# Performance work log

Hardware: AMD Instinct MI355X
Metric: run time of the kernel (lower is better)

## Reference

```python
import jax, jax.numpy as jnp
import numpy as np

# Mamba2 hyperparams derived from init_kwargs
D_MODEL = 512
FF = 2048
D_STATE = 128
D_CONV = 4
EXPAND = 2
D_INNER = EXPAND * D_MODEL          # 1024
HEADDIM = 64                        # mamba_ssm Mamba2 default
NHEADS = D_INNER // HEADDIM         # 16
NGROUPS = 1                         # default
CONV_DIM = D_INNER + 2 * NGROUPS * D_STATE      # 1280
D_IN_PROJ = 2 * D_INNER + 2 * NGROUPS * D_STATE + NHEADS  # 2320
B_SZ = 2
SEQ = 2048


def setup_inputs() -> dict:
    key = jax.random.key(0)
    ks = jax.random.split(key, 10)
    s = 0.02
    return dict(
        tgt=jax.random.normal(ks[0], (B_SZ, SEQ, D_MODEL), jnp.float32),
        W_in=jax.random.normal(ks[1], (D_MODEL, D_IN_PROJ), jnp.float32) * s,
        conv_w=jax.random.normal(ks[2], (CONV_DIM, D_CONV), jnp.float32) * s,
        conv_b=jnp.zeros((CONV_DIM,), jnp.float32),
        dt_bias=jax.random.uniform(ks[3], (NHEADS,), jnp.float32, -4.0, -1.0),
        A_log=jnp.log(jax.random.uniform(ks[4], (NHEADS,), jnp.float32, 1.0, 16.0)),
        D_skip=jnp.ones((NHEADS,), jnp.float32),
        gnorm_w=jnp.ones((D_INNER,), jnp.float32),
        W_out=jax.random.normal(ks[5], (D_INNER, D_MODEL), jnp.float32) * s,
        n1_g=jnp.ones((D_MODEL,), jnp.float32), n1_b=jnp.zeros((D_MODEL,), jnp.float32),
        ffn_w1=jax.random.normal(ks[6], (D_MODEL, FF), jnp.float32) * s,
        ffn_b1=jnp.zeros((FF,), jnp.float32),
        ffn_w2=jax.random.normal(ks[7], (FF, D_MODEL), jnp.float32) * s,
        ffn_b2=jnp.zeros((D_MODEL,), jnp.float32),
        n3_g=jnp.ones((D_MODEL,), jnp.float32), n3_b=jnp.zeros((D_MODEL,), jnp.float32),
    )


def _layernorm(x, g, b, eps=1e-5):
    m = jnp.mean(x, -1, keepdims=True)
    v = jnp.var(x, -1, keepdims=True)
    return (x - m) * jax.lax.rsqrt(v + eps) * g + b


def _mamba2(x, W_in, conv_w, conv_b, dt_bias, A_log, D_skip, gnorm_w, W_out):
    Bb, S, _ = x.shape
    zxbcdt = x @ W_in                               # (B,S,2320)
    z = zxbcdt[..., :D_INNER]                       # gate (B,S,1024)
    xBC = zxbcdt[..., D_INNER:D_INNER + CONV_DIM]   # (B,S,1280)
    dt = zxbcdt[..., D_INNER + CONV_DIM:]           # (B,S,H)
    # causal depthwise conv1d (kernel D_CONV) + SiLU
    xc = jnp.moveaxis(xBC, 1, 2)                    # (B,C,S)
    xp = jnp.pad(xc, ((0, 0), (0, 0), (D_CONV - 1, 0)))
    yc = sum(conv_w[None, :, k:k + 1] * xp[:, :, k:k + S] for k in range(D_CONV))
    xBC = jax.nn.silu(jnp.moveaxis(yc, 1, 2) + conv_b)
    xs = xBC[..., :D_INNER].reshape(Bb, S, NHEADS, HEADDIM)   # (B,S,H,P)
    Bc = xBC[..., D_INNER:D_INNER + D_STATE]                  # (B,S,N)
    Cc = xBC[..., D_INNER + D_STATE:]                         # (B,S,N)
    dt = jax.nn.softplus(dt + dt_bias)                        # (B,S,H)
    A = -jnp.exp(A_log)                                       # (H,)
    dA = jnp.exp(dt * A)                                      # (B,S,H)
    tm = lambda a: jnp.moveaxis(a, 1, 0)                      # time-major

    def step(h, inp):
        # h: (B,H,P,N) selective state
        dA_t, dt_t, B_t, C_t, x_t = inp
        h = h * dA_t[:, :, None, None] \
            + (dt_t[:, :, None] * x_t)[..., None] * B_t[:, None, None, :]
        y_t = jnp.einsum('bhpn,bn->bhp', h, C_t)
        return h, y_t

    h0 = jnp.zeros((Bb, NHEADS, HEADDIM, D_STATE), x.dtype)
    _, ys = jax.lax.scan(step, h0, (tm(dA), tm(dt), tm(Bc), tm(Cc), tm(xs)))
    y = jnp.moveaxis(ys, 0, 1) + D_skip[None, None, :, None] * xs
    y = y.reshape(Bb, S, D_INNER)
    # gated RMSNorm (norm_before_gate=False): norm(y * silu(z)) * w
    y = y * jax.nn.silu(z)
    y = y * jax.lax.rsqrt(jnp.mean(y * y, -1, keepdims=True) + 1e-5) * gnorm_w
    return y @ W_out


def reference(tgt, W_in, conv_w, conv_b, dt_bias, A_log, D_skip, gnorm_w, W_out,
              n1_g, n1_b, ffn_w1, ffn_b1, ffn_w2, ffn_b2, n3_g, n3_b):
    t = tgt + _mamba2(tgt, W_in, conv_w, conv_b, dt_bias, A_log, D_skip, gnorm_w, W_out)
    t = _layernorm(t, n1_g, n1_b)
    h = jax.nn.gelu(t @ ffn_w1 + ffn_b1, approximate=False) @ ffn_w2 + ffn_b2
    return _layernorm(t + h, n3_g, n3_b)
```

## Files before the change

### kernel.cpp

```cpp
#include <hip/hip_runtime.h>
#include <hip/hip_bf16.h>
#include <cstddef>
#include <cstdint>

#define D_MODEL   512
#define FF        2048
#define D_STATE   128
#define D_INNER   1024
#define HEADDIM   64
#define NHEADS    16
#define CONV_DIM  1280
#define D_IN_PROJ 2320
#define NPJ_PAD   2432
#define B_SZ      2
#define SEQ       2048
#define NTOK      (B_SZ*SEQ)
#define LCH       32
#define NCHUNK    (SEQ/LCH)
#define NCID      (B_SZ*NHEADS*NCHUNK)
#define LN_SLICE  ((size_t)NTOK*D_MODEL)

typedef __attribute__((ext_vector_type(8))) short short8;
typedef __attribute__((ext_vector_type(4))) float f32x4;

__device__ __forceinline__ float sigmoid_f(float x){ return 1.0f/(1.0f+expf(-x)); }
__device__ __forceinline__ float gelu_f(float x){ return 0.5f*x*(1.0f+erff(x*0.70710678118654752f)); }

__device__ __forceinline__ unsigned short bf16bits(float f){
  __hip_bfloat16 h = __float2bfloat16(f);
  return *reinterpret_cast<unsigned short*>(&h);
}
__device__ __forceinline__ float bf2f(unsigned short u){ return __uint_as_float(((unsigned)u)<<16); }
__device__ __forceinline__ float blo(unsigned u){ return __uint_as_float(u<<16); }
__device__ __forceinline__ float bhi(unsigned u){ return __uint_as_float(u & 0xffff0000u); }
__device__ __forceinline__ unsigned bfpack2(float a, float b){
  return (unsigned)bf16bits(a) | ((unsigned)bf16bits(b)<<16);
}

__device__ __forceinline__ void gload16(const void* g, void* l){
  __builtin_amdgcn_global_load_lds((const __attribute__((address_space(1))) void*)g,
                                   (__attribute__((address_space(3))) void*)l, 16, 0, 0);
}

union U4S8 { uint4 v; unsigned short s[8]; };

template<int EPI, typename OT>
__global__ __launch_bounds__(256)
void gemm128(const __hip_bfloat16* __restrict__ A, const __hip_bfloat16* __restrict__ Bt,
             const float* __restrict__ bias, OT* __restrict__ C,
             int N, int K, int ldc)
{
  __shared__ char AsRaw[128*128];
  __shared__ char BsRaw[128*128];

  const int t    = threadIdx.x;
  const int bm   = blockIdx.y * 128;
  const int bn   = blockIdx.x * 128;
  const int lane = t & 63;
  const int wid  = t >> 6;
  const int wr   = wid >> 1;
  const int wc   = wid & 1;
  const int lrow = lane & 15;
  const int lkb  = (lane >> 4) * 16;
  const int sw   = (lrow & 7) << 4;

  const int rA  = t >> 3;
  const int cbA = (t & 7) * 16;
  const int scb = cbA ^ ((rA & 7) << 4);
  const size_t strideA = (size_t)K * 2;
  const char* aSrc = (const char*)A  + (size_t)(bm + rA) * strideA + scb;
  const char* bSrc = (const char*)Bt + (size_t)(bn + rA) * strideA + scb;
  char* aDst = AsRaw + wid * 1024;
  char* bDst = BsRaw + wid * 1024;

  f32x4 acc[4][4];
  #pragma unroll
  for (int m=0;m<4;m++)
    #pragma unroll
    for (int n=0;n<4;n++) acc[m][n] = (f32x4){0.f,0.f,0.f,0.f};

  const char* ArP = AsRaw + (wr*64 + lrow) * 128;
  const char* BrP = BsRaw + (wc*64 + lrow) * 128;

  for (int k0 = 0; k0 < K; k0 += 64) {
    const size_t ko = (size_t)k0 * 2;
    gload16(aSrc + ko,               aDst);
    gload16(aSrc + ko + 32*strideA,  aDst + 4096);
    gload16(aSrc + ko + 64*strideA,  aDst + 8192);
    gload16(aSrc + ko + 96*strideA,  aDst + 12288);
    gload16(bSrc + ko,               bDst);
    gload16(bSrc + ko + 32*strideA,  bDst + 4096);
    gload16(bSrc + ko + 64*strideA,  bDst + 8192);
    gload16(bSrc + ko + 96*strideA,  bDst + 12288);
    __syncthreads();
    #pragma unroll
    for (int kk = 0; kk < 2; ++kk) {
      const int kb = (kk*64 + lkb) ^ sw;
      short8 a0 = *(const short8*)(ArP + 0*2048 + kb);
      short8 a1 = *(const short8*)(ArP + 1*2048 + kb);
      short8 a2 = *(const short8*)(ArP + 2*2048 + kb);
      short8 a3 = *(const short8*)(ArP + 3*2048 + kb);
      short8 b0 = *(const short8*)(BrP + 0*2048 + kb);
      short8 b1 = *(const short8*)(BrP + 1*2048 + kb);
      short8 b2 = *(const short8*)(BrP + 2*2048 + kb);
      short8 b3 = *(const short8*)(BrP + 3*2048 + kb);
      #pragma unroll
      for (int m=0;m<4;m++){
        short8 am = (m==0)?a0:(m==1)?a1:(m==2)?a2:a3;
        acc[m][0] = __builtin_amdgcn_mfma_f32_16x16x32_bf16(am, b0, acc[m][0], 0,0,0);
        acc[m][1] = __builtin_amdgcn_mfma_f32_16x16x32_bf16(am, b1, acc[m][1], 0,0,0);
        acc[m][2] = __builtin_amdgcn_mfma_f32_16x16x32_bf16(am, b2, acc[m][2], 0,0,0);
        acc[m][3] = __builtin_amdgcn_mfma_f32_16x16x32_bf16(am, b3, acc[m][3], 0,0,0);
      }
    }
    __syncthreads();
  }

  const int orow0 = bm + wr*64 + (lane >> 4) * 4;
  const int ocol0 = bn + wc*64 + lrow;
  #pragma unroll
  for (int n=0;n<4;n++) {
    const int col = ocol0 + n*16;
    if (col >= N) continue;
    const float bv = (EPI>=1) ? bias[col] : 0.f;
    #pragma unroll
    for (int m=0;m<4;m++) {
      #pragma unroll
      for (int j=0;j<4;j++) {
        float v = acc[m][n][j] + bv;
        if (EPI==2) v = gelu_f(v);
        OT* cp = C + (size_t)(orow0 + m*16 + j)*ldc + col;
        if constexpr (sizeof(OT)==2) *cp = __float2bfloat16(v); else *cp = v;
      }
    }
  }
}

template<int EPI, typename OT>
__global__ __launch_bounds__(256)
void gemm_bf16(const __hip_bfloat16* __restrict__ A, const __hip_bfloat16* __restrict__ Bt,
               const float* __restrict__ bias, OT* __restrict__ C,
               int N, int K, int ldc, int M, int nsplit)
{
  __shared__ char AsRaw[128*128];
  __shared__ char BsRaw[64*128];

  const int t    = threadIdx.x;
  const int bm   = blockIdx.y * 128;
  const int bn   = blockIdx.x * 64;
  const int z    = blockIdx.z;
  const int Kloop= K / nsplit;
  A += (size_t)z * Kloop;
  Bt += (size_t)z * Kloop;
  C += (size_t)z * M * ldc;

  const int lane = t & 63;
  const int wid  = t >> 6;
  const int wr   = wid >> 1;
  const int wc   = wid & 1;
  const int lrow = lane & 15;
  const int lkb  = (lane >> 4) * 16;
  const int sw   = (lrow & 7) << 4;

  const int rA  = t >> 3;
  const int cbA = (t & 7) * 16;
  const int scb = cbA ^ ((rA & 7) << 4);
  const size_t strideA = (size_t)K * 2;
  const char* aSrc = (const char*)A  + (size_t)(bm + rA) * strideA + scb;
  const char* bSrc = (const char*)Bt + (size_t)(bn + rA) * strideA + scb;
  char* aDst = AsRaw + wid * 1024;
  char* bDst = BsRaw + wid * 1024;

  f32x4 acc[4][2];
  #pragma unroll
  for (int m=0;m<4;m++)
    #pragma unroll
    for (int n=0;n<2;n++) acc[m][n] = (f32x4){0.f,0.f,0.f,0.f};

  const char* ArP = AsRaw + (wr*64 + lrow) * 128;
  const char* BrP = BsRaw + (wc*32 + lrow) * 128;

  for (int k0 = 0; k0 < Kloop; k0 += 64) {
    const size_t ko = (size_t)k0 * 2;
    gload16(aSrc + ko,               aDst);
    gload16(aSrc + ko + 32*strideA,  aDst + 4096);
    gload16(aSrc + ko + 64*strideA,  aDst + 8192);
    gload16(aSrc + ko + 96*strideA,  aDst + 12288);
    gload16(bSrc + ko,               bDst);
    gload16(bSrc + ko + 32*strideA,  bDst + 4096);
    __syncthreads();
    #pragma unroll
    for (int kk = 0; kk < 2; ++kk) {
      const int kb = (kk*64 + lkb) ^ sw;
      short8 a0 = *(const short8*)(ArP + 0*2048 + kb);
      short8 a1 = *(const short8*)(ArP + 1*2048 + kb);
      short8 a2 = *(const short8*)(ArP + 2*2048 + kb);
      short8 a3 = *(const short8*)(ArP + 3*2048 + kb);
      short8 b0 = *(const short8*)(BrP + 0*2048 + kb);
      short8 b1 = *(const short8*)(BrP + 1*2048 + kb);
      acc[0][0] = __builtin_amdgcn_mfma_f32_16x16x32_bf16(a0, b0, acc[0][0], 0,0,0);
      acc[1][0] = __builtin_amdgcn_mfma_f32_16x16x32_bf16(a1, b0, acc[1][0], 0,0,0);
      acc[2][0] = __builtin_amdgcn_mfma_f32_16x16x32_bf16(a2, b0, acc[2][0], 0,0,0);
      acc[3][0] = __builtin_amdgcn_mfma_f32_16x16x32_bf16(a3, b0, acc[3][0], 0,0,0);
      acc[0][1] = __builtin_amdgcn_mfma_f32_16x16x32_bf16(a0, b1, acc[0][1], 0,0,0);
      acc[1][1] = __builtin_amdgcn_mfma_f32_16x16x32_bf16(a1, b1, acc[1][1], 0,0,0);
      acc[2][1] = __builtin_amdgcn_mfma_f32_16x16x32_bf16(a2, b1, acc[2][1], 0,0,0);
      acc[3][1] = __builtin_amdgcn_mfma_f32_16x16x32_bf16(a3, b1, acc[3][1], 0,0,0);
    }
    __syncthreads();
  }

  const int orow0 = bm + wr*64 + (lane >> 4) * 4;
  const int ocol0 = bn + wc*32 + lrow;
  #pragma unroll
  for (int n=0;n<2;n++) {
    const int col = ocol0 + n*16;
    if (col >= N) continue;
    const float bv = (EPI>=1 && z==0) ? bias[col] : 0.f;
    #pragma unroll
    for (int m=0;m<4;m++) {
      #pragma unroll
      for (int j=0;j<4;j++) {
        float v = acc[m][n][j] + bv;
        if (EPI==2) v = gelu_f(v);
        OT* cp = C + (size_t)(orow0 + m*16 + j)*ldc + col;
        if constexpr (sizeof(OT)==2) *cp = __float2bfloat16(v); else *cp = v;
      }
    }
  }
}

__device__ __forceinline__ void tr_tile(const float* __restrict__ in,
                                        __hip_bfloat16* __restrict__ out,
                                        int K, int N, int Npad, int bx, int by)
{
  __shared__ float tbuf[32][33];
  const int tx = threadIdx.x & 31, ty = threadIdx.x >> 5;
  #pragma unroll
  for (int u=0;u<4;u++){
    int k = by*32 + ty + u*8;
    int n = bx*32 + tx;
    tbuf[ty+u*8][tx] = (n < N) ? in[(size_t)k*N + n] : 0.f;
  }
  __syncthreads();
  #pragma unroll
  for (int u=0;u<4;u++){
    int n = bx*32 + ty + u*8;
    int k = by*32 + tx;
    if (n < Npad) out[(size_t)n*K + k] = __float2bfloat16(tbuf[tx][ty+u*8]);
  }
}

__global__ __launch_bounds__(256)
void prep_all(const float* __restrict__ tgt, __hip_bfloat16* __restrict__ tgt_bf,
              const float* __restrict__ W_in,  __hip_bfloat16* __restrict__ Wint,
              const float* __restrict__ W_out, __hip_bfloat16* __restrict__ Woutt,
              const float* __restrict__ W1,    __hip_bfloat16* __restrict__ W1t,
              const float* __restrict__ W2,    __hip_bfloat16* __restrict__ W2t)
{
  int bid = blockIdx.x;
  if (bid < 2048) {
    int i = bid*1024 + threadIdx.x*4;
    float4 v = *(const float4*)(tgt + i);
    *(uint2*)(tgt_bf + i) = (uint2){bfpack2(v.x,v.y), bfpack2(v.z,v.w)};
    return;
  }
  bid -= 2048;
  if (bid < 76*16) { tr_tile(W_in, Wint, D_MODEL, D_IN_PROJ, NPJ_PAD, bid%76, bid/76); return; }
  bid -= 76*16;
  if (bid < 16*32) { tr_tile(W_out, Woutt, D_INNER, D_MODEL, D_MODEL, bid%16, bid/16); return; }
  bid -= 16*32;
  if (bid < 64*16) { tr_tile(W1, W1t, D_MODEL, FF, FF, bid%64, bid/64); return; }
  bid -= 64*16;
  tr_tile(W2, W2t, FF, D_MODEL, D_MODEL, bid%16, bid/16);
}

__global__ __launch_bounds__(256)
void conv_silu(const __hip_bfloat16* __restrict__ zx, const float* __restrict__ cw,
               const float* __restrict__ cb, __hip_bfloat16* __restrict__ xbc)
{
  const int c  = blockIdx.x*256 + threadIdx.x;
  const int t0 = blockIdx.y*64;
  const int b  = blockIdx.z;
  const float w0=cw[c*4+0], w1=cw[c*4+1], w2=cw[c*4+2], w3=cw[c*4+3];
  const float cbv = cb[c];
  const __hip_bfloat16* base = zx + ((size_t)(b*SEQ + t0))*D_IN_PROJ + D_INNER + c;
  __hip_bfloat16* obase = xbc + ((size_t)(b*SEQ + t0))*CONV_DIM + c;
  float xm3, xm2, xm1;
  if (t0 == 0) { xm3 = 0.f; xm2 = 0.f; xm1 = 0.f; }
  else {
    xm3 = __bfloat162float(base[-3*(ptrdiff_t)D_IN_PROJ]);
    xm2 = __bfloat162float(base[-2*(ptrdiff_t)D_IN_PROJ]);
    xm1 = __bfloat162float(base[-1*(ptrdiff_t)D_IN_PROJ]);
  }
  #pragma unroll 4
  for (int t=0; t<64; ++t) {
    float xc = __bfloat162float(base[(size_t)t*D_IN_PROJ]);
    float acc = cbv + w0*xm3 + w1*xm2 + w2*xm1 + w3*xc;
    obase[(size_t)t*CONV_DIM] = __float2bfloat16(acc * sigmoid_f(acc));
    xm3 = xm2; xm2 = xm1; xm1 = xc;
  }
}

__global__ __launch_bounds__(256)
void chunk_intra(const __hip_bfloat16* __restrict__ xbc, const __hip_bfloat16* __restrict__ zx,
                 const float* __restrict__ dt_bias,
                 const float* __restrict__ A_log, const float* __restrict__ D_skip,
                 __hip_bfloat16* __restrict__ y, __hip_bfloat16* __restrict__ Sbuf,
                 float* __restrict__ lcend, float* __restrict__ scl)
{
  __shared__ char sm[38912];
  __shared__ float s_dt[LCH], s_lc[LCH], s_wend[LCH];
  char* Cb  = sm;
  char* Bb  = sm + 8704;
  char* Btb = sm + 17408;
  char* Xtb = sm + 29696;
  char* Mb  = sm + 35840;

  const int cid = blockIdx.x;
  const int c  = cid & (NCHUNK-1);
  const int bh = cid >> 6;
  const int h  = bh & 15;
  const int b  = bh >> 4;
  const int tid = threadIdx.x;
  const int t0 = c*LCH;
  const __hip_bfloat16* rowbase = xbc + ((size_t)(b*SEQ + t0))*CONV_DIM;

  if (tid < 32) {
    float A_h = -expf(A_log[h]);
    float x = __bfloat162float(zx[(size_t)(b*SEQ + t0 + tid)*D_IN_PROJ + (D_INNER + CONV_DIM) + h])
              + dt_bias[h];
    float dtv = (x > 20.f) ? x : log1pf(expf(x));
    float lc = dtv * A_h;
    #pragma unroll
    for (int d=1; d<32; d<<=1) {
      float o = __shfl_up(lc, d, 32);
      if (tid >= d) lc += o;
    }
    float lc31 = __shfl(lc, 31, 32);
    s_dt[tid] = dtv;
    s_lc[tid] = lc;
    s_wend[tid] = expf(lc31 - lc) * dtv;
    scl[cid*LCH + tid] = expf(lc);
    if (tid == 31) lcend[cid] = lc;
  }

  #pragma unroll
  for (int u=0; u<2; ++u) {
    int q = tid + 256*u;
    int r = q >> 4, c8 = (q & 15)*8;
    const __hip_bfloat16* rp = rowbase + (size_t)r*CONV_DIM + D_INNER;
    *(uint4*)(Bb + r*272 + c8*2) = *(const uint4*)(rp + c8);
    *(uint4*)(Cb + r*272 + c8*2) = *(const uint4*)(rp + D_STATE + c8);
  }
  {
    int j = tid >> 3, p0 = (tid & 7)*8;
    U4S8 xv; xv.v = *(const uint4*)(rowbase + (size_t)j*CONV_DIM + h*HEADDIM + p0);
    #pragma unroll
    for (int k=0;k<8;k++)
      *(unsigned short*)(Xtb + ((p0+k)*48 + j)*2) = xv.s[k];
  }
  __syncthreads();

  #pragma unroll
  for (int u=0; u<2; ++u) {
    int q = tid + 256*u;
    int j = q >> 4, n8 = (q & 15)*8;
    const float w = s_wend[j];
    U4S8 bv; bv.v = *(const uint4*)(Bb + j*272 + n8*2);
    #pragma unroll
    for (int k=0;k<8;k++)
      *(unsigned short*)(Btb + ((n8+k)*48 + j)*2) = bf16bits(bf2f(bv.s[k]) * w);
  }

  const int lane = tid & 63;
  const int w    = tid >> 6;
  const int lrow = lane & 15;
  const int lkb  = (lane >> 4) * 16;
  {
    const int wi = w >> 1, wj = w & 1;
    f32x4 g = (f32x4){0.f,0.f,0.f,0.f};
    const char* Ar = Cb + (wi*16 + lrow)*272 + lkb;
    const char* Br = Bb + (wj*16 + lrow)*272 + lkb;
    #pragma unroll
    for (int ks=0; ks<4; ks++){
      short8 a  = *(const short8*)(Ar + ks*64);
      short8 bb = *(const short8*)(Br + ks*64);
      g = __builtin_amdgcn_mfma_f32_16x16x32_bf16(a, bb, g, 0,0,0);
    }
    const int j = wj*16 + lrow;
    const float lcj = s_lc[j], dtj = s_dt[j];
    const float dsk = D_skip[h];
    const int i0 = wi*16 + (lane>>4)*4;
    #pragma unroll
    for (int r=0;r<4;r++){
      int i = i0 + r;
      float m = 0.f;
      if (j <= i) { m = g[r]*expf(s_lc[i]-lcj)*dtj; if (j==i) m += dsk; }
      *(unsigned short*)(Mb + (i*48 + j)*2) = bf16bits(m);
    }
  }
  __syncthreads();

  {
    const int it = w >> 1;
    const int pb = (w & 1)*2;
    short8 am = *(const short8*)(Mb + (it*16+lrow)*96 + lkb);
    __hip_bfloat16* ybase = y + ((size_t)(b*SEQ+t0))*D_INNER + h*HEADDIM;
    #pragma unroll
    for (int pi=0; pi<2; pi++){
      short8 xv = *(const short8*)(Xtb + ((pb+pi)*16+lrow)*96 + lkb);
      f32x4 ya = __builtin_amdgcn_mfma_f32_16x16x32_bf16(am, xv, (f32x4){0.f,0.f,0.f,0.f}, 0,0,0);
      #pragma unroll
      for (int r=0;r<4;r++){
        int i = it*16 + (lane>>4)*4 + r;
        ybase[(size_t)i*D_INNER + (pb+pi)*16 + lrow] = __float2bfloat16(ya[r]);
      }
    }
  }

  f32x4 sacc[8];
  {
    short8 ax = *(const short8*)(Xtb + (w*16+lrow)*96 + lkb);
    #pragma unroll
    for (int nt=0;nt<8;nt++){
      short8 bv = *(const short8*)(Btb + (nt*16+lrow)*96 + lkb);
      sacc[nt] = __builtin_amdgcn_mfma_f32_16x16x32_bf16(ax, bv, (f32x4){0.f,0.f,0.f,0.f}, 0,0,0);
    }
  }
  __syncthreads();
  {
    const int p0b = w*16 + (lane>>4)*4;
    #pragma unroll
    for (int nt=0;nt<8;nt++){
      int n = nt*16 + lrow;
      #pragma unroll
      for (int r=0;r<4;r++)
        *(unsigned short*)(sm + (p0b+r)*272 + n*2) = bf16bits(sacc[nt][r]);
    }
  }
  __syncthreads();
  __hip_bfloat16* Sout = Sbuf + (size_t)cid*(D_STATE*HEADDIM);
  #pragma unroll
  for (int u=0;u<4;u++){
    int q = tid*4+u, row = q>>4, c8 = (q&15)*8;
    *(uint4*)(Sout + row*128 + c8) = *(const uint4*)(sm + row*272 + c8*2);
  }
}

__global__ __launch_bounds__(256)
void state_scan(__hip_bfloat16* __restrict__ Sbuf, const float* __restrict__ lcend)
{
  const int bh = blockIdx.x >> 2;
  const int sl = blockIdx.x & 3;
  const int tid = threadIdx.x;
  uint4* Sb4 = (uint4*)Sbuf;
  const int idx0 = bh*NCHUNK*1024 + sl*256 + tid;

  float H[8];
  #pragma unroll
  for (int r=0;r<8;r++) H[r]=0.f;
  uint4 cur = Sb4[idx0];
  uint4 nx1 = Sb4[idx0 + 1024];
  float lc0 = lcend[bh*NCHUNK];
  float lc1 = lcend[bh*NCHUNK + 1];
  for (int c=0;c<NCHUNK;c++){
    uint4 nx2; float lc2;
    if (c + 2 < NCHUNK) { nx2 = Sb4[idx0 + (c+2)*1024]; lc2 = lcend[bh*NCHUNK + c + 2]; }
    else                { nx2 = make_uint4(0,0,0,0);    lc2 = 0.f; }
    float e = expf(lc0);
    uint4 o;
    o.x = bfpack2(H[0],H[1]); o.y = bfpack2(H[2],H[3]);
    o.z = bfpack2(H[4],H[5]); o.w = bfpack2(H[6],H[7]);
    Sb4[idx0 + c*1024] = o;
    H[0]=e*H[0]+blo(cur.x); H[1]=e*H[1]+bhi(cur.x);
    H[2]=e*H[2]+blo(cur.y); H[3]=e*H[3]+bhi(cur.y);
    H[4]=e*H[4]+blo(cur.z); H[5]=e*H[5]+bhi(cur.z);
    H[6]=e*H[6]+blo(cur.w); H[7]=e*H[7]+bhi(cur.w);
    cur = nx1; nx1 = nx2; lc0 = lc1; lc1 = lc2;
  }
}

__global__ __launch_bounds__(256)
void chunk_inter(const __hip_bfloat16* __restrict__ xbc, const __hip_bfloat16* __restrict__ Sbuf,
                 const float* __restrict__ scl, __hip_bfloat16* __restrict__ y)
{
  __shared__ char sm2[8704 + 17408];
  __shared__ float s_scl[LCH];
  char* Cb = sm2;
  char* Ht = sm2 + 8704;
  const int cid = blockIdx.x;
  const int c  = cid & (NCHUNK-1);
  const int bh = cid >> 6;
  const int h  = bh & 15;
  const int b  = bh >> 4;
  const int tid = threadIdx.x;
  const int t0 = c*LCH;
  const __hip_bfloat16* rowbase = xbc + ((size_t)(b*SEQ + t0))*CONV_DIM;

  #pragma unroll
  for (int u=0;u<2;u++){
    int q = tid + 256*u;
    int r = q >> 4, c8 = (q & 15)*8;
    *(uint4*)(Cb + r*272 + c8*2) = *(const uint4*)(rowbase + (size_t)r*CONV_DIM + D_INNER + D_STATE + c8);
  }
  const uint4* Hin = (const uint4*)(Sbuf + (size_t)cid*(D_STATE*HEADDIM));
  #pragma unroll
  for (int u=0;u<4;u++){
    int q = tid*4+u, row = q>>4, c8 = (q&15)*8;
    *(uint4*)(Ht + row*272 + c8*2) = Hin[q];
  }
  if (tid < 32) s_scl[tid] = scl[cid*LCH + tid];
  __syncthreads();

  const int lane = tid & 63;
  const int w    = tid >> 6;
  const int lrow = lane & 15;
  const int lkb  = (lane >> 4) * 16;
  const int it   = w >> 1;
  const int pb   = (w & 1)*2;
  f32x4 acc[2];
  acc[0] = (f32x4){0.f,0.f,0.f,0.f};
  acc[1] = (f32x4){0.f,0.f,0.f,0.f};
  const char* Ar = Cb + (it*16+lrow)*272 + lkb;
  const char* H0 = Ht + ((pb+0)*16+lrow)*272 + lkb;
  const char* H1 = Ht + ((pb+1)*16+lrow)*272 + lkb;
  #pragma unroll
  for (int ks=0; ks<4; ks++){
    short8 a  = *(const short8*)(Ar + ks*64);
    short8 h0 = *(const short8*)(H0 + ks*64);
    short8 h1 = *(const short8*)(H1 + ks*64);
    acc[0] = __builtin_amdgcn_mfma_f32_16x16x32_bf16(a, h0, acc[0], 0,0,0);
    acc[1] = __builtin_amdgcn_mfma_f32_16x16x32_bf16(a, h1, acc[1], 0,0,0);
  }
  __hip_bfloat16* ybase = y + ((size_t)(b*SEQ+t0))*D_INNER + h*HEADDIM;
  #pragma unroll
  for (int pi=0; pi<2; pi++){
    #pragma unroll
    for (int r=0;r<4;r++){
      int i = it*16 + (lane>>4)*4 + r;
      __hip_bfloat16* yp = ybase + (size_t)i*D_INNER + (pb+pi)*16 + lrow;
      float v = __bfloat162float(*yp) + s_scl[i]*acc[pi][r];
      *yp = __float2bfloat16(v);
    }
  }
}

__global__ __launch_bounds__(256)
void gate_rms(const __hip_bfloat16* __restrict__ zx, const float* __restrict__ gw,
              const __hip_bfloat16* __restrict__ yin, __hip_bfloat16* __restrict__ ybf)
{
  int tok = blockIdx.x;
  int c = threadIdx.x*4;
  uint2 zv2 = *(const uint2*)(zx + (size_t)tok*D_IN_PROJ + c);
  uint2 yv2 = *(const uint2*)(yin + (size_t)tok*D_INNER + c);
  float z0 = blo(zv2.x), z1 = bhi(zv2.x), z2 = blo(zv2.y), z3 = bhi(zv2.y);
  float y0 = blo(yv2.x), y1 = bhi(yv2.x), y2 = blo(yv2.y), y3 = bhi(yv2.y);
  float g0 = y0 * (z0 * sigmoid_f(z0));
  float g1 = y1 * (z1 * sigmoid_f(z1));
  float g2 = y2 * (z2 * sigmoid_f(z2));
  float g3 = y3 * (z3 * sigmoid_f(z3));
  float ss = g0*g0 + g1*g1 + g2*g2 + g3*g3;
  #pragma unroll
  for (int m=32;m>=1;m>>=1) ss += __shfl_xor(ss, m, 64);
  __shared__ float red[4];
  int wv = threadIdx.x >> 6;
  if ((threadIdx.x & 63)==0) red[wv]=ss;
  __syncthreads();
  float tot = red[0]+red[1]+red[2]+red[3];
  float sc = rsqrtf(tot*(1.f/1024.f) + 1e-5f);
  float4 gwv = *(const float4*)(gw + c);
  *(uint2*)(ybf + (size_t)tok*D_INNER + c) =
      (uint2){bfpack2(g0*sc*gwv.x, g1*sc*gwv.y), bfpack2(g2*sc*gwv.z, g3*sc*gwv.w)};
}

template<int WBF, int NS>
__global__ __launch_bounds__(256)
void add_ln(const float* __restrict__ a, const float* __restrict__ bres,
            const float* __restrict__ gg, const float* __restrict__ bb,
            float* __restrict__ out, __hip_bfloat16* __restrict__ outbf)
{
  int tok = blockIdx.x;
  size_t o = (size_t)tok*D_MODEL;
  int c0 = threadIdx.x, c1 = threadIdx.x + 256;
  float v0 = bres[o+c0];
  float v1 = bres[o+c1];
  #pragma unroll
  for (int z=0; z<NS; ++z) {
    v0 += a[o + z*LN_SLICE + c0];
    v1 += a[o + z*LN_SLICE + c1];
  }
  float s = v0+v1, sq = v0*v0+v1*v1;
  #pragma unroll
  for (int m=32;m>=1;m>>=1){ s += __shfl_xor(s,m,64); sq += __shfl_xor(sq,m,64); }
  __shared__ float rs[4], rq[4];
  int wv = threadIdx.x>>6;
  if ((threadIdx.x&63)==0){ rs[wv]=s; rq[wv]=sq; }
  __syncthreads();
  float S = rs[0]+rs[1]+rs[2]+rs[3];
  float Q = rq[0]+rq[1]+rq[2]+rq[3];
  float mean = S*(1.f/512.f);
  float var  = Q*(1.f/512.f) - mean*mean;
  float inv  = rsqrtf(var + 1e-5f);
  float o0 = (v0-mean)*inv*gg[c0] + bb[c0];
  float o1 = (v1-mean)*inv*gg[c1] + bb[c1];
  out[o+c0] = o0;
  out[o+c1] = o1;
  if (WBF) { outbf[o+c0] = __float2bfloat16(o0); outbf[o+c1] = __float2bfloat16(o1); }
}

extern "C" void kernel_launch(void* const* d_in, const int* in_sizes, int n_in,
                              void* d_out, int out_size, void* d_ws, size_t ws_size,
                              hipStream_t stream)
{
  const float* tgt    = (const float*)d_in[0];
  const float* W_in   = (const float*)d_in[1];
  const float* conv_w = (const float*)d_in[2];
  const float* conv_b = (const float*)d_in[3];
  const float* dt_bias= (const float*)d_in[4];
  const float* A_log  = (const float*)d_in[5];
  const float* D_skip = (const float*)d_in[6];
  const float* gnorm_w= (const float*)d_in[7];
  const float* W_out  = (const float*)d_in[8];
  const float* n1_g   = (const float*)d_in[9];
  const float* n1_b   = (const float*)d_in[10];
  const float* ffn_w1 = (const float*)d_in[11];
  const float* ffn_b1 = (const float*)d_in[12];
  const float* ffn_w2 = (const float*)d_in[13];
  const float* ffn_b2 = (const float*)d_in[14];
  const float* n3_g   = (const float*)d_in[15];
  const float* n3_b   = (const float*)d_in[16];
  float* out = (float*)d_out;
  float* ws  = (float*)d_ws;

  float* zxF  = ws;
  __hip_bfloat16* zx = (__hip_bfloat16*)zxF;
  float* xbcF = zxF + (size_t)NTOK*D_IN_PROJ;
  __hip_bfloat16* xbc = (__hip_bfloat16*)xbcF;
  float* ybF  = xbcF + 2621440 + 65536;
  __hip_bfloat16* yb = (__hip_bfloat16*)ybF;
  float* Sreg = ybF + 4194304;
  __hip_bfloat16* Sbuf = (__hip_bfloat16*)Sreg;
  float* lcend= Sreg + 8388608;
  float* scl  = lcend + NCID;
  float* wreg = scl + 65536;
  __hip_bfloat16* Wint  = (__hip_bfloat16*)wreg;
  __hip_bfloat16* Woutt = (__hip_bfloat16*)(wreg + 622592);
  __hip_bfloat16* W1t   = (__hip_bfloat16*)(wreg + 622592+262144);
  __hip_bfloat16* W2t   = (__hip_bfloat16*)(wreg + 622592+262144+524288);
  __hip_bfloat16* tgt_bf= (__hip_bfloat16*)(wreg + 622592+262144+524288+524288);
  float* tmp  = wreg + 622592+262144+524288+524288+1048576;

  __hip_bfloat16* yb_bf = (__hip_bfloat16*)xbcF;
  __hip_bfloat16* tb_bf = (__hip_bfloat16*)ybF;
  float* tb   = Sreg;
  __hip_bfloat16* hmid_bf = (__hip_bfloat16*)zxF;

  prep_all<<<2048 + 76*16 + 16*32 + 64*16 + 16*64, 256, 0, stream>>>(
      tgt, tgt_bf, W_in, Wint, W_out, Woutt, ffn_w1, W1t, ffn_w2, W2t);
  gemm128<0,__hip_bfloat16><<<dim3(NPJ_PAD/128, NTOK/128), 256, 0, stream>>>(
      tgt_bf, Wint, nullptr, zx, D_IN_PROJ, D_MODEL, D_IN_PROJ);
  conv_silu<<<dim3(CONV_DIM/256, SEQ/64, B_SZ), 256, 0, stream>>>(zx, conv_w, conv_b, xbc);
  chunk_intra<<<NCID, 256, 0, stream>>>(xbc, zx, dt_bias, A_log, D_skip, yb, Sbuf, lcend, scl);
  state_scan<<<B_SZ*NHEADS*4, 256, 0, stream>>>(Sbuf, lcend);
  chunk_inter<<<NCID, 256, 0, stream>>>(xbc, Sbuf, scl, yb);
  gate_rms<<<NTOK, 256, 0, stream>>>(zx, gnorm_w, yb, yb_bf);
  gemm_bf16<0,float><<<dim3(D_MODEL/64, NTOK/128, 2), 256, 0, stream>>>(
      yb_bf, Woutt, nullptr, tmp, D_MODEL, D_INNER, D_MODEL, NTOK, 2);
  add_ln<1,2><<<NTOK, 256, 0, stream>>>(tmp, tgt, n1_g, n1_b, tb, tb_bf);
  gemm128<2,__hip_bfloat16><<<dim3(FF/128, NTOK/128), 256, 0, stream>>>(
      tb_bf, W1t, ffn_b1, hmid_bf, FF, D_MODEL, FF);
  gemm_bf16<1,float><<<dim3(D_MODEL/64, NTOK/128, 2), 256, 0, stream>>>(
      hmid_bf, W2t, ffn_b2, tmp, D_MODEL, FF, D_MODEL, NTOK, 2);
  add_ln<0,2><<<NTOK, 256, 0, stream>>>(tmp, tb, n3_g, n3_b, out, nullptr);
}
```

Baseline: 174.3 us.

## Fuse causal conv1d+SiLU into chunk_intra and chunk_inter, drop xbc buffer

Removes the standalone conv_silu kernel and its intermediate xbc buffer. Each chunk block now computes the depthwise conv and SiLU for the channels it needs (its head's x slice, and B and C) directly from zx and writes them into shared memory. The aim is to save a kernel launch and the global write and read of xbc. In exchange, B and C are recomputed redundantly by all 16 heads, with C recomputed again in chunk_inter, and only 160 or 64 threads do serial 32-step loops with narrow 4-byte strided loads.

```diff
diff --git a/kernel.cpp b/kernel.cpp
--- a/kernel.cpp
+++ b/kernel.cpp
@@ -276,34 +276,8 @@
 }
 
 __global__ __launch_bounds__(256)
-void conv_silu(const __hip_bfloat16* __restrict__ zx, const float* __restrict__ cw,
-               const float* __restrict__ cb, __hip_bfloat16* __restrict__ xbc)
-{
-  const int c  = blockIdx.x*256 + threadIdx.x;
-  const int t0 = blockIdx.y*64;
-  const int b  = blockIdx.z;
-  const float w0=cw[c*4+0], w1=cw[c*4+1], w2=cw[c*4+2], w3=cw[c*4+3];
-  const float cbv = cb[c];
-  const __hip_bfloat16* base = zx + ((size_t)(b*SEQ + t0))*D_IN_PROJ + D_INNER + c;
-  __hip_bfloat16* obase = xbc + ((size_t)(b*SEQ + t0))*CONV_DIM + c;
-  float xm3, xm2, xm1;
-  if (t0 == 0) { xm3 = 0.f; xm2 = 0.f; xm1 = 0.f; }
-  else {
-    xm3 = __bfloat162float(base[-3*(ptrdiff_t)D_IN_PROJ]);
-    xm2 = __bfloat162float(base[-2*(ptrdiff_t)D_IN_PROJ]);
-    xm1 = __bfloat162float(base[-1*(ptrdiff_t)D_IN_PROJ]);
-  }
-  #pragma unroll 4
-  for (int t=0; t<64; ++t) {
-    float xc = __bfloat162float(base[(size_t)t*D_IN_PROJ]);
-    float acc = cbv + w0*xm3 + w1*xm2 + w2*xm1 + w3*xc;
-    obase[(size_t)t*CONV_DIM] = __float2bfloat16(acc * sigmoid_f(acc));
-    xm3 = xm2; xm2 = xm1; xm1 = xc;
-  }
-}
-
-__global__ __launch_bounds__(256)
-void chunk_intra(const __hip_bfloat16* __restrict__ xbc, const __hip_bfloat16* __restrict__ zx,
+void chunk_intra(const __hip_bfloat16* __restrict__ zx,
+                 const float* __restrict__ cw, const float* __restrict__ cb,
                  const float* __restrict__ dt_bias,
                  const float* __restrict__ A_log, const float* __restrict__ D_skip,
                  __hip_bfloat16* __restrict__ y, __hip_bfloat16* __restrict__ Sbuf,
@@ -324,7 +298,6 @@
   const int b  = bh >> 4;
   const int tid = threadIdx.x;
   const int t0 = c*LCH;
-  const __hip_bfloat16* rowbase = xbc + ((size_t)(b*SEQ + t0))*CONV_DIM;
 
   if (tid < 32) {
     float A_h = -expf(A_log[h]);
@@ -345,20 +318,39 @@
     if (tid == 31) lcend[cid] = lc;
   }
 
-  #pragma unroll
-  for (int u=0; u<2; ++u) {
-    int q = tid + 256*u;
-    int r = q >> 4, c8 = (q & 15)*8;
-    const __hip_bfloat16* rp = rowbase + (size_t)r*CONV_DIM + D_INNER;
-    *(uint4*)(Bb + r*272 + c8*2) = *(const uint4*)(rp + c8);
-    *(uint4*)(Cb + r*272 + c8*2) = *(const uint4*)(rp + D_STATE + c8);
-  }
-  {
-    int j = tid >> 3, p0 = (tid & 7)*8;
-    U4S8 xv; xv.v = *(const uint4*)(rowbase + (size_t)j*CONV_DIM + h*HEADDIM + p0);
-    #pragma unroll
-    for (int k=0;k<8;k++)
-      *(unsigned short*)(Xtb + ((p0+k)*48 + j)*2) = xv.s[k];
+  if (tid < 160) {
+    int loc, cc0, kind;
+    if (tid < 32)      { kind=0; loc = tid*2;       cc0 = h*HEADDIM + loc; }
+    else if (tid < 96) { kind=1; loc = (tid-32)*2;  cc0 = 1024 + loc; }
+    else               { kind=2; loc = (tid-96)*2;  cc0 = 1152 + loc; }
+    float4 wA = *(const float4*)(cw + (size_t)cc0*4);
+    float4 wB = *(const float4*)(cw + (size_t)cc0*4 + 4);
+    float cbA = cb[cc0], cbB = cb[cc0+1];
+    const __hip_bfloat16* zb = zx + ((size_t)(b*SEQ + t0))*D_IN_PROJ + D_INNER + cc0;
+    float pa3,pa2,pa1, pb3,pb2,pb1;
+    if (c == 0) { pa3=pa2=pa1=pb3=pb2=pb1=0.f; }
+    else {
+      unsigned v3 = *(const unsigned*)(zb - 3*(ptrdiff_t)D_IN_PROJ);
+      unsigned v2 = *(const unsigned*)(zb - 2*(ptrdiff_t)D_IN_PROJ);
+      unsigned v1 = *(const unsigned*)(zb - 1*(ptrdiff_t)D_IN_PROJ);
+      pa3=blo(v3); pb3=bhi(v3); pa2=blo(v2); pb2=bhi(v2); pa1=blo(v1); pb1=bhi(v1);
+    }
+    char* dstrow = (kind==1) ? Bb : Cb;
+    #pragma unroll 4
+    for (int r=0; r<32; ++r) {
+      unsigned vc = *(const unsigned*)(zb + (size_t)r*D_IN_PROJ);
+      float ca = blo(vc), cb2 = bhi(vc);
+      float oa = cbA + wA.x*pa3 + wA.y*pa2 + wA.z*pa1 + wA.w*ca;
+      float ob = cbB + wB.x*pb3 + wB.y*pb2 + wB.z*pb1 + wB.w*cb2;
+      oa = oa * sigmoid_f(oa); ob = ob * sigmoid_f(ob);
+      if (kind == 0) {
+        *(unsigned short*)(Xtb + ((loc  )*48 + r)*2) = bf16bits(oa);
+        *(unsigned short*)(Xtb + ((loc+1)*48 + r)*2) = bf16bits(ob);
+      } else {
+        *(unsigned*)(dstrow + r*272 + loc*2) = bfpack2(oa, ob);
+      }
+      pa3=pa2; pa2=pa1; pa1=ca; pb3=pb2; pb2=pb1; pb1=cb2;
+    }
   }
   __syncthreads();
 
@@ -482,7 +474,9 @@
 }
 
 __global__ __launch_bounds__(256)
-void chunk_inter(const __hip_bfloat16* __restrict__ xbc, const __hip_bfloat16* __restrict__ Sbuf,
+void chunk_inter(const __hip_bfloat16* __restrict__ zx,
+                 const float* __restrict__ cw, const float* __restrict__ cb,
+                 const __hip_bfloat16* __restrict__ Sbuf,
                  const float* __restrict__ scl, __hip_bfloat16* __restrict__ y)
 {
   __shared__ char sm2[8704 + 17408];
@@ -496,13 +490,32 @@
   const int b  = bh >> 4;
   const int tid = threadIdx.x;
   const int t0 = c*LCH;
-  const __hip_bfloat16* rowbase = xbc + ((size_t)(b*SEQ + t0))*CONV_DIM;
-
-  #pragma unroll
-  for (int u=0;u<2;u++){
-    int q = tid + 256*u;
-    int r = q >> 4, c8 = (q & 15)*8;
-    *(uint4*)(Cb + r*272 + c8*2) = *(const uint4*)(rowbase + (size_t)r*CONV_DIM + D_INNER + D_STATE + c8);
+
+  if (tid < 64) {
+    int loc = tid*2;
+    int cc0 = 1152 + loc;
+    float4 wA = *(const float4*)(cw + (size_t)cc0*4);
+    float4 wB = *(const float4*)(cw + (size_t)cc0*4 + 4);
+    float cbA = cb[cc0], cbB = cb[cc0+1];
+    const __hip_bfloat16* zb = zx + ((size_t)(b*SEQ + t0))*D_IN_PROJ + D_INNER + cc0;
+    float pa3,pa2,pa1, pb3,pb2,pb1;
+    if (c == 0) { pa3=pa2=pa1=pb3=pb2=pb1=0.f; }
+    else {
+      unsigned v3 = *(const unsigned*)(zb - 3*(ptrdiff_t)D_IN_PROJ);
+      unsigned v2 = *(const unsigned*)(zb - 2*(ptrdiff_t)D_IN_PROJ);
+      unsigned v1 = *(const unsigned*)(zb - 1*(ptrdiff_t)D_IN_PROJ);
+      pa3=blo(v3); pb3=bhi(v3); pa2=blo(v2); pb2=bhi(v2); pa1=blo(v1); pb1=bhi(v1);
+    }
+    #pragma unroll 4
+    for (int r=0; r<32; ++r) {
+      unsigned vc = *(const unsigned*)(zb + (size_t)r*D_IN_PROJ);
+      float ca = blo(vc), cb2 = bhi(vc);
+      float oa = cbA + wA.x*pa3 + wA.y*pa2 + wA.z*pa1 + wA.w*ca;
+      float ob = cbB + wB.x*pb3 + wB.y*pb2 + wB.z*pb1 + wB.w*cb2;
+      oa = oa * sigmoid_f(oa); ob = ob * sigmoid_f(ob);
+      *(unsigned*)(Cb + r*272 + loc*2) = bfpack2(oa, ob);
+      pa3=pa2; pa2=pa1; pa1=ca; pb3=pb2; pb2=pb1; pb1=cb2;
+    }
   }
   const uint4* Hin = (const uint4*)(Sbuf + (size_t)cid*(D_STATE*HEADDIM));
   #pragma unroll
@@ -636,7 +649,6 @@
   float* zxF  = ws;
   __hip_bfloat16* zx = (__hip_bfloat16*)zxF;
   float* xbcF = zxF + (size_t)NTOK*D_IN_PROJ;
-  __hip_bfloat16* xbc = (__hip_bfloat16*)xbcF;
   float* ybF  = xbcF + 2621440 + 65536;
   __hip_bfloat16* yb = (__hip_bfloat16*)ybF;
   float* Sreg = ybF + 4194304;
@@ -660,10 +672,10 @@
       tgt, tgt_bf, W_in, Wint, W_out, Woutt, ffn_w1, W1t, ffn_w2, W2t);
   gemm128<0,__hip_bfloat16><<<dim3(NPJ_PAD/128, NTOK/128), 256, 0, stream>>>(
       tgt_bf, Wint, nullptr, zx, D_IN_PROJ, D_MODEL, D_IN_PROJ);
-  conv_silu<<<dim3(CONV_DIM/256, SEQ/64, B_SZ), 256, 0, stream>>>(zx, conv_w, conv_b, xbc);
-  chunk_intra<<<NCID, 256, 0, stream>>>(xbc, zx, dt_bias, A_log, D_skip, yb, Sbuf, lcend, scl);
+  chunk_intra<<<NCID, 256, 0, stream>>>(zx, conv_w, conv_b, dt_bias, A_log, D_skip,
+                                        yb, Sbuf, lcend, scl);
   state_scan<<<B_SZ*NHEADS*4, 256, 0, stream>>>(Sbuf, lcend);
-  chunk_inter<<<NCID, 256, 0, stream>>>(xbc, Sbuf, scl, yb);
+  chunk_inter<<<NCID, 256, 0, stream>>>(zx, conv_w, conv_b, Sbuf, scl, yb);
   gate_rms<<<NTOK, 256, 0, stream>>>(zx, gnorm_w, yb, yb_bf);
   gemm_bf16<0,float><<<dim3(D_MODEL/64, NTOK/128, 2), 256, 0, stream>>>(
       yb_bf, Woutt, nullptr, tmp, D_MODEL, D_INNER, D_MODEL, NTOK, 2);
```

Result: slower. 200.3 us (+14.9%).
